# Optimization experiments

Measured on AMD Instinct MI355X. Metric: run time of the kernel, lower is better.

The kernel has to match this reference:

```python
import jax, jax.numpy as jnp
import numpy as np

B, T, C, H, D = 128, 256, 384, 6, 64  # batch, seq (block_size), embed, heads, head_size


def setup_inputs() -> dict:
    key = jax.random.key(0)
    ks = jax.random.split(key, 6)
    s = 0.02  # init scale
    return {
        "x": jax.random.normal(ks[0], (B, T, C), dtype=jnp.float32),
        "wq": jax.random.normal(ks[1], (H, C, D), dtype=jnp.float32) * s,
        "wk": jax.random.normal(ks[2], (H, C, D), dtype=jnp.float32) * s,
        "wv": jax.random.normal(ks[3], (H, C, D), dtype=jnp.float32) * s,
        "wp": jax.random.normal(ks[4], (H * D, C), dtype=jnp.float32) * s,
        "bp": jax.random.normal(ks[5], (C,), dtype=jnp.float32) * s,
    }


def reference(x, wq, wk, wv, wp, bp):
    # Batched multi-head causal self-attention (eval mode: dropout = identity).
    Bx, Tx, Cx = x.shape
    q = jnp.einsum("btc,hcd->bhtd", x, wq)
    k = jnp.einsum("btc,hcd->bhtd", x, wk)
    v = jnp.einsum("btc,hcd->bhtd", x, wv)
    scale = jnp.asarray(D, x.dtype) ** -0.5
    scores = jnp.einsum("bhtd,bhsd->bhts", q, k) * scale
    mask = jnp.tril(jnp.ones((Tx, Tx), dtype=bool))  # causal
    scores = jnp.where(mask, scores, -jnp.inf)
    w = jax.nn.softmax(scores, axis=-1)
    out = jnp.einsum("bhts,bhsd->bhtd", w, v)
    out = out.transpose(0, 2, 1, 3).reshape(Bx, Tx, H * D)  # concat heads
    return out @ wp + bp
```

## Files before the change

kernel.cpp:

```cpp
#include <hip/hip_runtime.h>
#include <hip/hip_bf16.h>

typedef __bf16 bf16x8 __attribute__((ext_vector_type(8)));
typedef __bf16 bf16x4 __attribute__((ext_vector_type(4)));
typedef float  f32x4  __attribute__((ext_vector_type(4)));

#define MFMA16(a,b,c) __builtin_amdgcn_mfma_f32_16x16x32_bf16((a),(b),(c),0,0,0)

static constexpr int Tt = 256;
static constexpr int Cc = 384;
static constexpr int Hh = 6;
static constexpr int Dd = 64;
static constexpr int HD = 384;
static constexpr int NQ = 1152;

__device__ __forceinline__ void gload16(const void* g, void* l) {
  __builtin_amdgcn_global_load_lds(
      (const __attribute__((address_space(1))) void*)g,
      (__attribute__((address_space(3))) void*)l, 16, 0, 0);
}

__global__ __launch_bounds__(256) void xcast(
    const float* __restrict__ x, __bf16* __restrict__ xb)
{
  size_t i = (size_t)blockIdx.x * 256 + threadIdx.x;
  const float4* p = (const float4*)(x + i * 8);
  float4 a = p[0], b = p[1];
  bf16x8 o;
  o[0] = (__bf16)a.x; o[1] = (__bf16)a.y; o[2] = (__bf16)a.z; o[3] = (__bf16)a.w;
  o[4] = (__bf16)b.x; o[5] = (__bf16)b.y; o[6] = (__bf16)b.z; o[7] = (__bf16)b.w;
  *(bf16x8*)(xb + i * 8) = o;
}

__global__ __launch_bounds__(256) void prep_w(
    const float* __restrict__ wq, const float* __restrict__ wk,
    const float* __restrict__ wv, const float* __restrict__ wp,
    __bf16* __restrict__ wqkvb, __bf16* __restrict__ wpb)
{
  int idx = blockIdx.x * 256 + threadIdx.x;
  const int n1 = NQ * Cc;
  if (idx < n1) {
    int n = idx / Cc, c = idx % Cc;
    int which = n / HD, r = n % HD, h = r >> 6, d = r & 63;
    const float* w = which == 0 ? wq : (which == 1 ? wk : wv);
    wqkvb[idx] = (__bf16)w[(h * Cc + c) * Dd + d];
  } else {
    int j = idx - n1;
    if (j < Cc * HD) {
      int co = j / HD, ci = j % HD;
      wpb[j] = (__bf16)wp[ci * Cc + co];
    }
  }
}

__global__ __launch_bounds__(256) void gemm_qkv(
    const __bf16* __restrict__ xb, const __bf16* __restrict__ wn,
    __bf16* __restrict__ qkv, int Mc)
{
  __shared__ __align__(16) char smem[36864];
  char* Al = smem;
  char* Bl = smem + 16384;

  const int tid = threadIdx.x;
  const int m0 = blockIdx.x * 128;
  const int n0 = blockIdx.y * 128;
  const int wid = tid >> 6, ln = tid & 63;
  const int wm = wid >> 1, wn_ = wid & 1;
  const int lr = ln & 15, lg = ln >> 4;
  const int srow = ln >> 3, sslot = ln & 7;

  f32x4 acc[4][4];
#pragma unroll
  for (int i = 0; i < 4; ++i)
#pragma unroll
    for (int j = 0; j < 4; ++j) acc[i][j] = f32x4{0.f, 0.f, 0.f, 0.f};

  for (int kt = 0; kt < Cc; kt += 64) {
#pragma unroll
    for (int i = 0; i < 4; ++i) {
      int off = (wid * 4 + i) << 10;
      int row = (off >> 7) + srow;
      gload16(xb + (size_t)(m0 + row) * Cc + kt + ((sslot ^ (row & 7)) << 3), Al + off);
    }
#pragma unroll
    for (int i = 0; i < 4; ++i) {
      int off = (wid * 4 + i) << 10;
      int row = (off >> 7) + srow;
      gload16(wn + (size_t)(n0 + row) * Cc + kt + ((sslot ^ (row & 7)) << 3), Bl + off);
    }
    __syncthreads();
#pragma unroll
    for (int ks = 0; ks < 2; ++ks) {
      bf16x8 af[4], bfr[4];
#pragma unroll
      for (int mi = 0; mi < 4; ++mi) {
        int r = wm * 64 + mi * 16 + lr;
        af[mi] = *(const bf16x8*)(Al + r * 128 + (((ks * 4 + lg) ^ (r & 7)) << 4));
      }
#pragma unroll
      for (int ni = 0; ni < 4; ++ni) {
        int r = wn_ * 64 + ni * 16 + lr;
        bfr[ni] = *(const bf16x8*)(Bl + r * 128 + (((ks * 4 + lg) ^ (r & 7)) << 4));
      }
      __builtin_amdgcn_s_setprio(1);
#pragma unroll
      for (int mi = 0; mi < 4; ++mi)
#pragma unroll
        for (int ni = 0; ni < 4; ++ni)
          acc[mi][ni] = MFMA16(af[mi], bfr[ni], acc[mi][ni]);
      __builtin_amdgcn_s_setprio(0);
    }
    __syncthreads();
  }

  __bf16* Cl = (__bf16*)smem;
#pragma unroll
  for (int mi = 0; mi < 4; ++mi)
#pragma unroll
    for (int ni = 0; ni < 4; ++ni)
#pragma unroll
      for (int j = 0; j < 4; ++j) {
        int row = wm * 64 + mi * 16 + lg * 4 + j;
        int col = wn_ * 64 + ni * 16 + lr;
        *((__bf16*)((char*)Cl + row * 272 + col * 2)) = (__bf16)acc[mi][ni][j];
      }
  __syncthreads();
#pragma unroll
  for (int p = 0; p < 8; ++p) {
    int row = p * 16 + (tid >> 4);
    int ch = tid & 15;
    bf16x8 v = *(const bf16x8*)((char*)Cl + row * 272 + ch * 16);
    int m = m0 + row, n = n0 + ch * 8;
    int which = n / HD, r = n % HD, h = r >> 6, d = r & 63;
    int bl = m >> 8, t = m & 255;
    *(bf16x8*)(qkv + (size_t)which * ((size_t)Mc * HD) +
               ((size_t)(bl * Hh + h) * Tt + t) * Dd + d) = v;
  }
}

__global__ __launch_bounds__(512) void attn_k(
    const __bf16* __restrict__ q, const __bf16* __restrict__ k,
    const __bf16* __restrict__ v, __bf16* __restrict__ att)
{
  __shared__ __align__(16) char smem[131072];
  char* Kl = smem;
  char* Vl = smem + 32768;
  char* Pl = smem + 65536;

  const int bh = blockIdx.x;
  const int tid = threadIdx.x, wid = tid >> 6, lane = tid & 63;
  const int lr = lane & 15, lg = lane >> 4;
  const size_t base = (size_t)bh * (Tt * Dd);

#pragma unroll
  for (int i = 0; i < 4; ++i) {
    int off = (wid * 4 + i) << 10;
    int row = (off >> 7) + (lane >> 3);
    int slot = lane & 7;
    gload16(k + base + row * 64 + ((slot ^ (row & 7)) << 3), Kl + off);
  }
#pragma unroll
  for (int i = 0; i < 4; ++i) {
    int chunk = tid + 512 * i;
    int key = chunk >> 3, d8 = chunk & 7;
    bf16x8 vv = *(const bf16x8*)(v + base + key * 64 + d8 * 8);
#pragma unroll
    for (int e = 0; e < 8; ++e) {
      int d = d8 * 8 + e;
      *(__bf16*)(Vl + ((d * 512 + key * 2) ^ ((d & 7) << 4))) = vv[e];
    }
  }
  __syncthreads();

  char* Pw = Pl + wid * 8192;
  const int bl = bh / Hh, h = bh % Hh;

  for (int qi = 0; qi < 2; ++qi) {
    const int qt = qi == 0 ? wid : 15 - wid;
    const int qbase = qt * 16;

    bf16x8 qf0 = *(const bf16x8*)(q + base + (qbase + lr) * 64 + lg * 8);
    bf16x8 qf1 = *(const bf16x8*)(q + base + (qbase + lr) * 64 + 32 + lg * 8);

    f32x4 s[16];
#pragma unroll
    for (int n = 0; n < 16; ++n) s[n] = f32x4{0.f, 0.f, 0.f, 0.f};
    __builtin_amdgcn_s_setprio(1);
#pragma unroll
    for (int n = 0; n < 16; ++n) {
      if (n <= qt) {
        int rowb = (n * 16 + lr) * 128;
        int swz = (lr & 7) << 4;
        bf16x8 k0 = *(const bf16x8*)(Kl + ((rowb + lg * 16) ^ swz));
        bf16x8 k1 = *(const bf16x8*)(Kl + ((rowb + 64 + lg * 16) ^ swz));
        s[n] = MFMA16(qf0, k0, s[n]);
        s[n] = MFMA16(qf1, k1, s[n]);
      }
    }
    __builtin_amdgcn_s_setprio(0);
#pragma unroll
    for (int n = 0; n < 16; ++n)
#pragma unroll
      for (int j = 0; j < 4; ++j) {
        int key = n * 16 + lr;
        int qrow = qbase + lg * 4 + j;
        s[n][j] = (n <= qt && key <= qrow) ? s[n][j] * 0.125f : -1e30f;
      }
    float m4[4] = {-1e30f, -1e30f, -1e30f, -1e30f};
#pragma unroll
    for (int n = 0; n < 16; ++n)
#pragma unroll
      for (int j = 0; j < 4; ++j) m4[j] = fmaxf(m4[j], s[n][j]);
#pragma unroll
    for (int j = 0; j < 4; ++j) {
      m4[j] = fmaxf(m4[j], __shfl_xor(m4[j], 1));
      m4[j] = fmaxf(m4[j], __shfl_xor(m4[j], 2));
      m4[j] = fmaxf(m4[j], __shfl_xor(m4[j], 4));
      m4[j] = fmaxf(m4[j], __shfl_xor(m4[j], 8));
    }
    float sum4[4] = {0.f, 0.f, 0.f, 0.f};
#pragma unroll
    for (int n = 0; n < 16; ++n)
#pragma unroll
      for (int j = 0; j < 4; ++j) {
        float p = __expf(s[n][j] - m4[j]);
        s[n][j] = p;
        sum4[j] += p;
      }
#pragma unroll
    for (int j = 0; j < 4; ++j) {
      sum4[j] += __shfl_xor(sum4[j], 1);
      sum4[j] += __shfl_xor(sum4[j], 2);
      sum4[j] += __shfl_xor(sum4[j], 4);
      sum4[j] += __shfl_xor(sum4[j], 8);
    }
    float inv4[4];
#pragma unroll
    for (int j = 0; j < 4; ++j) inv4[j] = 1.0f / sum4[j];

#pragma unroll
    for (int j = 0; j < 4; ++j) {
      int ql = lg * 4 + j;
      int rswz = (ql & 7) << 4;
#pragma unroll
      for (int n = 0; n < 16; ++n) {
        float p = s[n][j] * inv4[j];
        *(__bf16*)(Pw + ((ql * 512 + (n * 16 + lr) * 2) ^ rswz)) = (__bf16)p;
      }
    }
    asm volatile("s_waitcnt lgkmcnt(0)" ::: "memory");

    f32x4 o[4];
#pragma unroll
    for (int dn = 0; dn < 4; ++dn) o[dn] = f32x4{0.f, 0.f, 0.f, 0.f};
    const int kkmax = (qbase + 15) >> 5;
    __builtin_amdgcn_s_setprio(1);
#pragma unroll
    for (int kk = 0; kk < 8; ++kk) {
      if (kk <= kkmax) {
        bf16x8 pa = *(const bf16x8*)(Pw + ((lr * 512 + kk * 64 + lg * 16) ^ ((lr & 7) << 4)));
#pragma unroll
        for (int dn = 0; dn < 4; ++dn) {
          int d = dn * 16 + lr;
          bf16x8 vb = *(const bf16x8*)(Vl + ((d * 512 + kk * 64 + lg * 16) ^ ((d & 7) << 4)));
          o[dn] = MFMA16(pa, vb, o[dn]);
        }
      }
    }
    __builtin_amdgcn_s_setprio(0);
#pragma unroll
    for (int dn = 0; dn < 4; ++dn)
#pragma unroll
      for (int j = 0; j < 4; ++j) {
        int qrow = qbase + lg * 4 + j;
        att[((size_t)(bl * Tt + qrow)) * HD + h * Dd + dn * 16 + lr] = (__bf16)o[dn][j];
      }
  }
}

__global__ __launch_bounds__(256) void gemm_out(
    const __bf16* __restrict__ att, const __bf16* __restrict__ wpb,
    const float* __restrict__ bp, float* __restrict__ out, int Mc)
{
  __shared__ __align__(16) char smem[32768];
  char* Al = smem;
  char* Bl = smem + 16384;

  const int tid = threadIdx.x;
  const int m0 = blockIdx.x * 128;
  const int n0 = blockIdx.y * 128;
  const int wid = tid >> 6, ln = tid & 63;
  const int wm = wid >> 1, wn_ = wid & 1;
  const int lr = ln & 15, lg = ln >> 4;
  const int srow = ln >> 3, sslot = ln & 7;

  f32x4 acc[4][4];
#pragma unroll
  for (int i = 0; i < 4; ++i)
#pragma unroll
    for (int j = 0; j < 4; ++j) acc[i][j] = f32x4{0.f, 0.f, 0.f, 0.f};

  for (int kt = 0; kt < Cc; kt += 64) {
#pragma unroll
    for (int i = 0; i < 4; ++i) {
      int off = (wid * 4 + i) << 10;
      int row = (off >> 7) + srow;
      gload16(att + (size_t)(m0 + row) * Cc + kt + ((sslot ^ (row & 7)) << 3), Al + off);
    }
#pragma unroll
    for (int i = 0; i < 4; ++i) {
      int off = (wid * 4 + i) << 10;
      int row = (off >> 7) + srow;
      gload16(wpb + (size_t)(n0 + row) * Cc + kt + ((sslot ^ (row & 7)) << 3), Bl + off);
    }
    __syncthreads();
#pragma unroll
    for (int ks = 0; ks < 2; ++ks) {
      bf16x8 af[4], bfr[4];
#pragma unroll
      for (int mi = 0; mi < 4; ++mi) {
        int r = wm * 64 + mi * 16 + lr;
        af[mi] = *(const bf16x8*)(Al + r * 128 + (((ks * 4 + lg) ^ (r & 7)) << 4));
      }
#pragma unroll
      for (int ni = 0; ni < 4; ++ni) {
        int r = wn_ * 64 + ni * 16 + lr;
        bfr[ni] = *(const bf16x8*)(Bl + r * 128 + (((ks * 4 + lg) ^ (r & 7)) << 4));
      }
      __builtin_amdgcn_s_setprio(1);
#pragma unroll
      for (int mi = 0; mi < 4; ++mi)
#pragma unroll
        for (int ni = 0; ni < 4; ++ni)
          acc[mi][ni] = MFMA16(af[mi], bfr[ni], acc[mi][ni]);
      __builtin_amdgcn_s_setprio(0);
    }
    __syncthreads();
  }
#pragma unroll
  for (int ni = 0; ni < 4; ++ni) {
    int n = n0 + wn_ * 64 + ni * 16 + lr;
    float bv = bp[n];
#pragma unroll
    for (int mi = 0; mi < 4; ++mi)
#pragma unroll
      for (int j = 0; j < 4; ++j) {
        int m = m0 + wm * 64 + mi * 16 + lg * 4 + j;
        out[(size_t)m * Cc + n] = acc[mi][ni][j] + bv;
      }
  }
}

extern "C" void kernel_launch(void* const* d_in, const int* in_sizes, int n_in,
                              void* d_out, int out_size, void* d_ws, size_t ws_size,
                              hipStream_t stream) {
  const float* x  = (const float*)d_in[0];
  const float* wq = (const float*)d_in[1];
  const float* wk = (const float*)d_in[2];
  const float* wv = (const float*)d_in[3];
  const float* wp = (const float*)d_in[4];
  const float* bp = (const float*)d_in[5];
  float* out = (float*)d_out;

  char* ws = (char*)d_ws;
  __bf16* wqkvb = (__bf16*)ws;
  __bf16* wpb   = (__bf16*)(ws + 884736);
  char*   dyn   = ws + 1179648;

  int Bc = 128;
  while (Bc > 1 && 1179648ull + (unsigned long long)Bc * 786432ull > (unsigned long long)ws_size)
    Bc >>= 1;
  const int Mc = Bc * 256;
  __bf16* xb  = (__bf16*)dyn;
  __bf16* att = xb;
  __bf16* qkv = (__bf16*)(dyn + (size_t)Mc * HD * 2);

  prep_w<<<2304, 256, 0, stream>>>(wq, wk, wv, wp, wqkvb, wpb);

  for (int b0 = 0; b0 < 128; b0 += Bc) {
    const float* xc  = x + (size_t)b0 * Tt * Cc;
    float* outc      = out + (size_t)b0 * Tt * Cc;
    xcast<<<Bc * 48, 256, 0, stream>>>(xc, xb);
    gemm_qkv<<<dim3(Mc / 128, 9), 256, 0, stream>>>(xb, wqkvb, qkv, Mc);
    attn_k<<<Bc * Hh, 512, 0, stream>>>(qkv, qkv + (size_t)Mc * HD,
                                        qkv + (size_t)2 * Mc * HD, att);
    gemm_out<<<dim3(Mc / 128, 3), 256, 0, stream>>>(att, wpb, bp, outc, Mc);
  }
}
```

Measured before the change: 218.5 us.

## Keep attention probabilities in registers via transposed QK and lane shuffles

The QK^T MFMA now computes S transposed, so each lane holds one query column and the softmax max and sum reduce with two cross-lane shuffles instead of four. Probabilities are packed to bf16 in registers and rearranged into the PV operand layout with __shfl, which removes the per-wave LDS P buffer and its scattered scalar stores. Normalization is deferred to the output write. LDS use halves to 64KB and launch bounds request more occupancy, at the cost of many extra shuffle instructions in the PV loop.

```diff
diff --git a/kernel.cpp b/kernel.cpp
--- a/kernel.cpp
+++ b/kernel.cpp
@@ -4,6 +4,7 @@
 typedef __bf16 bf16x8 __attribute__((ext_vector_type(8)));
 typedef __bf16 bf16x4 __attribute__((ext_vector_type(4)));
 typedef float  f32x4  __attribute__((ext_vector_type(4)));
+typedef int    i32x4  __attribute__((ext_vector_type(4)));
 
 #define MFMA16(a,b,c) __builtin_amdgcn_mfma_f32_16x16x32_bf16((a),(b),(c),0,0,0)
 
@@ -138,14 +139,13 @@
   }
 }
 
-__global__ __launch_bounds__(512) void attn_k(
+__global__ __launch_bounds__(512, 4) void attn_k(
     const __bf16* __restrict__ q, const __bf16* __restrict__ k,
     const __bf16* __restrict__ v, __bf16* __restrict__ att)
 {
-  __shared__ __align__(16) char smem[131072];
+  __shared__ __align__(128) char smem[65536];
   char* Kl = smem;
   char* Vl = smem + 32768;
-  char* Pl = smem + 65536;
 
   const int bh = blockIdx.x;
   const int tid = threadIdx.x, wid = tid >> 6, lane = tid & 63;
@@ -172,11 +172,10 @@
   }
   __syncthreads();
 
-  char* Pw = Pl + wid * 8192;
   const int bl = bh / Hh, h = bh % Hh;
 
   for (int qi = 0; qi < 2; ++qi) {
-    const int qt = qi == 0 ? wid : 15 - wid;
+    const int qt = (qi == 0) ? wid : 15 - wid;
     const int qbase = qt * 16;
 
     bf16x8 qf0 = *(const bf16x8*)(q + base + (qbase + lr) * 64 + lg * 8);
@@ -193,88 +192,92 @@
         int swz = (lr & 7) << 4;
         bf16x8 k0 = *(const bf16x8*)(Kl + ((rowb + lg * 16) ^ swz));
         bf16x8 k1 = *(const bf16x8*)(Kl + ((rowb + 64 + lg * 16) ^ swz));
-        s[n] = MFMA16(qf0, k0, s[n]);
-        s[n] = MFMA16(qf1, k1, s[n]);
+        s[n] = MFMA16(k0, qf0, s[n]);
+        s[n] = MFMA16(k1, qf1, s[n]);
       }
     }
     __builtin_amdgcn_s_setprio(0);
-#pragma unroll
-    for (int n = 0; n < 16; ++n)
-#pragma unroll
-      for (int j = 0; j < 4; ++j) {
-        int key = n * 16 + lr;
-        int qrow = qbase + lg * 4 + j;
-        s[n][j] = (n <= qt && key <= qrow) ? s[n][j] * 0.125f : -1e30f;
-      }
-    float m4[4] = {-1e30f, -1e30f, -1e30f, -1e30f};
-#pragma unroll
-    for (int n = 0; n < 16; ++n)
-#pragma unroll
-      for (int j = 0; j < 4; ++j) m4[j] = fmaxf(m4[j], s[n][j]);
-#pragma unroll
-    for (int j = 0; j < 4; ++j) {
-      m4[j] = fmaxf(m4[j], __shfl_xor(m4[j], 1));
-      m4[j] = fmaxf(m4[j], __shfl_xor(m4[j], 2));
-      m4[j] = fmaxf(m4[j], __shfl_xor(m4[j], 4));
-      m4[j] = fmaxf(m4[j], __shfl_xor(m4[j], 8));
-    }
-    float sum4[4] = {0.f, 0.f, 0.f, 0.f};
-#pragma unroll
-    for (int n = 0; n < 16; ++n)
-#pragma unroll
-      for (int j = 0; j < 4; ++j) {
-        float p = __expf(s[n][j] - m4[j]);
-        s[n][j] = p;
-        sum4[j] += p;
-      }
-#pragma unroll
-    for (int j = 0; j < 4; ++j) {
-      sum4[j] += __shfl_xor(sum4[j], 1);
-      sum4[j] += __shfl_xor(sum4[j], 2);
-      sum4[j] += __shfl_xor(sum4[j], 4);
-      sum4[j] += __shfl_xor(sum4[j], 8);
-    }
-    float inv4[4];
-#pragma unroll
-    for (int j = 0; j < 4; ++j) inv4[j] = 1.0f / sum4[j];
-
-#pragma unroll
-    for (int j = 0; j < 4; ++j) {
-      int ql = lg * 4 + j;
-      int rswz = (ql & 7) << 4;
-#pragma unroll
-      for (int n = 0; n < 16; ++n) {
-        float p = s[n][j] * inv4[j];
-        *(__bf16*)(Pw + ((ql * 512 + (n * 16 + lr) * 2) ^ rswz)) = (__bf16)p;
-      }
-    }
-    asm volatile("s_waitcnt lgkmcnt(0)" ::: "memory");
+
+    float mx = -1e30f;
+#pragma unroll
+    for (int n = 0; n < 16; ++n) {
+      if (n <= qt) {
+#pragma unroll
+        for (int j = 0; j < 4; ++j) {
+          float sv = s[n][j] * 0.125f;
+          if (n == qt && 4 * lg + j > lr) sv = -1e30f;
+          s[n][j] = sv;
+          mx = fmaxf(mx, sv);
+        }
+      }
+    }
+    mx = fmaxf(mx, __shfl_xor(mx, 16));
+    mx = fmaxf(mx, __shfl_xor(mx, 32));
+
+    float sum = 0.f;
+    int w[16][2];
+#pragma unroll
+    for (int n = 0; n < 16; ++n) {
+      if (n <= qt) {
+        float e0 = __expf(s[n][0] - mx);
+        float e1 = __expf(s[n][1] - mx);
+        float e2 = __expf(s[n][2] - mx);
+        float e3 = __expf(s[n][3] - mx);
+        sum += (e0 + e1) + (e2 + e3);
+        union { __bf16 hh[2]; int ii; } u0, u1;
+        u0.hh[0] = (__bf16)e0; u0.hh[1] = (__bf16)e1;
+        u1.hh[0] = (__bf16)e2; u1.hh[1] = (__bf16)e3;
+        w[n][0] = u0.ii;
+        w[n][1] = u1.ii;
+      } else if (n == (qt | 1)) {
+        w[n][0] = 0; w[n][1] = 0;
+      }
+    }
+    sum += __shfl_xor(sum, 16);
+    sum += __shfl_xor(sum, 32);
+    float inv = 1.0f / sum;
 
     f32x4 o[4];
 #pragma unroll
     for (int dn = 0; dn < 4; ++dn) o[dn] = f32x4{0.f, 0.f, 0.f, 0.f};
-    const int kkmax = (qbase + 15) >> 5;
-    __builtin_amdgcn_s_setprio(1);
+    const int kkmax = qt >> 1;
 #pragma unroll
     for (int kk = 0; kk < 8; ++kk) {
       if (kk <= kkmax) {
-        bf16x8 pa = *(const bf16x8*)(Pw + ((lr * 512 + kk * 64 + lg * 16) ^ ((lr & 7) << 4)));
+        int s0 = lr + ((lg & 1) << 5);
+        int s1 = s0 + 16;
+        int hi = lg >> 1;
+        int a0 = __shfl(w[2 * kk][0], s0), b0 = __shfl(w[2 * kk + 1][0], s0);
+        int a1 = __shfl(w[2 * kk][1], s0), b1 = __shfl(w[2 * kk + 1][1], s0);
+        int a2 = __shfl(w[2 * kk][0], s1), b2 = __shfl(w[2 * kk + 1][0], s1);
+        int a3 = __shfl(w[2 * kk][1], s1), b3 = __shfl(w[2 * kk + 1][1], s1);
+        i32x4 pwv;
+        pwv[0] = hi ? b0 : a0;
+        pwv[1] = hi ? b1 : a1;
+        pwv[2] = hi ? b2 : a2;
+        pwv[3] = hi ? b3 : a3;
+        bf16x8 pa = __builtin_bit_cast(bf16x8, pwv);
+
+        __builtin_amdgcn_s_setprio(1);
 #pragma unroll
         for (int dn = 0; dn < 4; ++dn) {
           int d = dn * 16 + lr;
           bf16x8 vb = *(const bf16x8*)(Vl + ((d * 512 + kk * 64 + lg * 16) ^ ((d & 7) << 4)));
           o[dn] = MFMA16(pa, vb, o[dn]);
         }
-      }
-    }
-    __builtin_amdgcn_s_setprio(0);
-#pragma unroll
-    for (int dn = 0; dn < 4; ++dn)
-#pragma unroll
-      for (int j = 0; j < 4; ++j) {
-        int qrow = qbase + lg * 4 + j;
-        att[((size_t)(bl * Tt + qrow)) * HD + h * Dd + dn * 16 + lr] = (__bf16)o[dn][j];
-      }
+        __builtin_amdgcn_s_setprio(0);
+      }
+    }
+
+#pragma unroll
+    for (int j = 0; j < 4; ++j) {
+      float invj = __shfl(inv, lg * 4 + j, 16);
+      int qrow = qbase + lg * 4 + j;
+#pragma unroll
+      for (int dn = 0; dn < 4; ++dn)
+        att[((size_t)(bl * Tt + qrow)) * HD + h * Dd + dn * 16 + lr] =
+            (__bf16)(o[dn][j] * invj);
+    }
   }
 }
 
```

Result: slower. 278.3 us (+27.4%).
